# Kernel optimization log

Measured on AMD Instinct MI355X. Metric: run time of the kernel, lower is better.

Reference implementation:

```python
import jax, jax.numpy as jnp
import numpy as np

NUM_SCALES = 3
LAMBDA_0 = 1.0
MU_0 = 1.0
KAPPA_LAMBDA = 0.5
KAPPA_MU = 0.5
BASE_WEIGHT = 1.0
GRADIENT_SCALING = 0.1


def tgradient(f, axis):
    """torch.gradient semantics: central diff interior, one-sided at edges (spacing=1)."""
    n = f.shape[axis]
    def sl(a, b):
        idx = [slice(None)] * f.ndim
        idx[axis] = slice(a, b)
        return f[tuple(idx)]
    interior = (sl(2, n) - sl(0, n - 2)) * 0.5
    first = sl(1, 2) - sl(0, 1)
    last = sl(n - 1, n) - sl(n - 2, n - 1)
    return jnp.concatenate([first, interior, last], axis=axis)


def resize1d_linear(x, axis, out_size):
    """1D linear resize along `axis` with align_corners=True."""
    in_size = x.shape[axis]
    if out_size == in_size:
        return x
    denom = max(out_size - 1, 1)
    coords = jnp.arange(out_size, dtype=jnp.float32) * ((in_size - 1) / denom)
    i0 = jnp.floor(coords).astype(jnp.int32)
    i1 = jnp.minimum(i0 + 1, in_size - 1)
    w = (coords - i0.astype(jnp.float32)).astype(x.dtype)
    shape = [1] * x.ndim
    shape[axis] = out_size
    w = w.reshape(shape)
    x0 = jnp.take(x, i0, axis=axis)
    x1 = jnp.take(x, i1, axis=axis)
    return x0 * (1 - w) + x1 * w


def trilinear_downsample(x, scale):
    # F.interpolate(..., scale_factor=1/scale, mode='trilinear', align_corners=True,
    # recompute_scale_factor=True): out_size = floor(in_size / scale); separable linear.
    for axis in (2, 3, 4):
        out_size = int(np.floor(x.shape[axis] / scale))
        x = resize1d_linear(x, axis, out_size)
    return x


def elasticity_loss(deformation_field, image):
    total_loss = jnp.float32(0.0)
    for i in range(NUM_SCALES):
        scale = 2 ** i
        deform = trilinear_downsample(deformation_field, scale)
        img = trilinear_downsample(image, scale)
        u, v, w = deform[:, 0], deform[:, 1], deform[:, 2]  # each (B, X, Y, Z)
        du_dx, du_dy, du_dz = tgradient(u, 1), tgradient(u, 2), tgradient(u, 3)
        dv_dx, dv_dy, dv_dz = tgradient(v, 1), tgradient(v, 2), tgradient(v, 3)
        dw_dx, dw_dy, dw_dz = tgradient(w, 1), tgradient(w, 2), tgradient(w, 3)
        E_xx, E_yy, E_zz = du_dx, dv_dy, dw_dz
        E_xy = 0.5 * (du_dy + dv_dx)
        E_xz = 0.5 * (du_dz + dw_dx)
        E_yz = 0.5 * (dv_dz + dw_dy)
        trace_E = E_xx + E_yy + E_zz
        ic = img[:, 0]  # (B, X, Y, Z)
        gx, gy, gz = tgradient(ic, 1), tgradient(ic, 2), tgradient(ic, 3)
        image_gradient = jnp.sqrt(gx * gx + gy * gy + gz * gz)
        adaptive_lambda = LAMBDA_0 + KAPPA_LAMBDA * image_gradient
        adaptive_mu = MU_0 + KAPPA_MU * image_gradient
        elastic_energy = (0.5 * adaptive_lambda * trace_E ** 2
                          + adaptive_mu * (E_xx ** 2 + E_yy ** 2 + E_zz ** 2
                                           + 2.0 * (E_xy ** 2 + E_xz ** 2 + E_yz ** 2)))
        adaptive_weight = BASE_WEIGHT + GRADIENT_SCALING * image_gradient
        total_loss = total_loss + jnp.mean(adaptive_weight * elastic_energy)
    return total_loss


def setup_inputs() -> dict:
    key = jax.random.key(0)
    k1, k2 = jax.random.split(key)
    deformation_field = jax.random.normal(k1, (2, 3, 160, 192, 160), dtype=jnp.float32)
    image = jax.random.uniform(k2, (2, 1, 160, 192, 160), dtype=jnp.float32)
    return {"deformation_field": deformation_field, "image": image}


def reference(deformation_field, image):
    return elasticity_loss(deformation_field, image)
```

## Files before the change

kernel.cpp:

```cpp
#include <hip/hip_runtime.h>
#include <math.h>


#define LAMBDA_0 1.0f
#define MU_0 1.0f
#define KAPPA_LAMBDA 0.5f
#define KAPPA_MU 0.5f
#define BASE_WEIGHT 1.0f
#define GRADIENT_SCALING 0.1f

typedef float v4f __attribute__((ext_vector_type(4)));

constexpr int S_TY = 32;
constexpr int S_TZ = 32;
constexpr int S_CX = 8;

__global__ __launch_bounds__(256, 2)
void elasticity_stream_reg2_kernel(const float* __restrict__ def,
                                   const float* __restrict__ img,
                                   int X, int Y, int Z,
                                   int nby, int nbz, int nbx,
                                   float inv_n, float* __restrict__ out) {
    int t = blockIdx.x;
    const int bx = t % nbx; t /= nbx;
    const int bz = t % nbz; t /= nbz;
    const int by = t % nby; t /= nby;
    const int b = t;

    const int tid = threadIdx.x;
    const int zg = tid & 7;
    const int ly = tid >> 3;
    const int lane = tid & 63;
    const int laneM = (lane - 1) & 63;
    const int laneP = (lane + 1) & 63;

    const long long vol = (long long)X * Y * Z;
    const long long sX = (long long)Y * Z;
    const float* __restrict__ p0 = def + ((long long)b * 3 + 0) * vol;
    const float* __restrict__ p1 = def + ((long long)b * 3 + 1) * vol;
    const float* __restrict__ p2 = def + ((long long)b * 3 + 2) * vol;
    const float* __restrict__ p3 = img + (long long)b * vol;

    const int gy = by * S_TY + ly;
    const int gz0 = bz * S_TZ + 4 * zg;
    const int x0 = bx * S_CX;

    const long long offC  = (long long)gy * Z + gz0;
    const long long offYm = (long long)max(gy - 1, 0) * Z + gz0;
    const long long offYp = (long long)min(gy + 1, Y - 1) * Z + gz0;
    const long long offZm = offC - ((gz0 > 0) ? 1 : 0);
    const long long offZp = offC + ((gz0 + 4 < Z) ? 4 : 3);

    const bool ylo = (gy == 0), yhi = (gy == Y - 1);
    const bool zlo = (gz0 == 0), zhi = (gz0 + 4 == Z);
    const bool zem = (zg == 0),  zep = (zg == 7);

    v4f pc[4], cc[4], nc[4];
    {
        const long long o_ = (long long)max(x0 - 1, 0) * sX;
        pc[0] = *(const v4f*)(p0 + o_ + offC);
        pc[1] = *(const v4f*)(p1 + o_ + offC);
        pc[2] = *(const v4f*)(p2 + o_ + offC);
        pc[3] = *(const v4f*)(p3 + o_ + offC);
    }
    {
        const long long o_ = (long long)x0 * sX;
        cc[0] = *(const v4f*)(p0 + o_ + offC);
        cc[1] = *(const v4f*)(p1 + o_ + offC);
        cc[2] = *(const v4f*)(p2 + o_ + offC);
        cc[3] = *(const v4f*)(p3 + o_ + offC);
    }

    float acc = 0.f;
#pragma unroll 2
    for (int i = 0; i < S_CX; ++i) {
        const int x = x0 + i;
        const bool xlo = (x == 0), xhi = (x == X - 1);
        const long long oC = (long long)x * sX;
        const long long oN = (long long)min(x + 1, X - 1) * sX;

        nc[0] = *(const v4f*)(p0 + oN + offC);
        nc[1] = *(const v4f*)(p1 + oN + offC);
        nc[2] = *(const v4f*)(p2 + oN + offC);
        nc[3] = *(const v4f*)(p3 + oN + offC);

        v4f ym[4], yp[4];
        ym[0] = *(const v4f*)(p0 + oC + offYm);
        ym[1] = *(const v4f*)(p1 + oC + offYm);
        ym[2] = *(const v4f*)(p2 + oC + offYm);
        ym[3] = *(const v4f*)(p3 + oC + offYm);
        yp[0] = *(const v4f*)(p0 + oC + offYp);
        yp[1] = *(const v4f*)(p1 + oC + offYp);
        yp[2] = *(const v4f*)(p2 + oC + offYp);
        yp[3] = *(const v4f*)(p3 + oC + offYp);

        float zmS[4] = {0.f, 0.f, 0.f, 0.f};
        float zpS[4] = {0.f, 0.f, 0.f, 0.f};
        if (zem) {
            zmS[0] = p0[oC + offZm]; zmS[1] = p1[oC + offZm];
            zmS[2] = p2[oC + offZm]; zmS[3] = p3[oC + offZm];
        }
        if (zep) {
            zpS[0] = p0[oC + offZp]; zpS[1] = p1[oC + offZp];
            zpS[2] = p2[oC + offZp]; zpS[3] = p3[oC + offZp];
        }

        v4f gxA[4], gyA[4], gzA[4];
#pragma unroll
        for (int f = 0; f < 4; ++f) {
            v4f c = cc[f];
            gxA[f] = xlo ? (nc[f] - c)
                         : (xhi ? (c - pc[f]) : 0.5f * (nc[f] - pc[f]));
            gyA[f] = ylo ? (yp[f] - c)
                         : (yhi ? (c - ym[f]) : 0.5f * (yp[f] - ym[f]));
            float zmv = __shfl(c[3], laneM, 64);
            float zpv = __shfl(c[0], laneP, 64);
            float zm = zem ? zmS[f] : zmv;
            float zp = zep ? zpS[f] : zpv;
            v4f gz;
            gz[0] = zlo ? (c[1] - c[0]) : 0.5f * (c[1] - zm);
            gz[1] = 0.5f * (c[2] - c[0]);
            gz[2] = 0.5f * (c[3] - c[1]);
            gz[3] = zhi ? (c[3] - c[2]) : 0.5f * (zp - c[2]);
            gzA[f] = gz;
        }

#pragma unroll
        for (int j = 0; j < 4; ++j) {
            float Exx = gxA[0][j], Eyy = gyA[1][j], Ezz = gzA[2][j];
            float Exy = 0.5f * (gyA[0][j] + gxA[1][j]);
            float Exz = 0.5f * (gzA[0][j] + gxA[2][j]);
            float Eyz = 0.5f * (gzA[1][j] + gyA[2][j]);
            float tr = Exx + Eyy + Ezz;
            float g = sqrtf(gxA[3][j] * gxA[3][j] + gyA[3][j] * gyA[3][j] +
                            gzA[3][j] * gzA[3][j]);
            float lam = LAMBDA_0 + KAPPA_LAMBDA * g;
            float mu  = MU_0 + KAPPA_MU * g;
            float energy = 0.5f * lam * tr * tr +
                           mu * (Exx * Exx + Eyy * Eyy + Ezz * Ezz +
                                 2.0f * (Exy * Exy + Exz * Exz + Eyz * Eyz));
            acc += (BASE_WEIGHT + GRADIENT_SCALING * g) * energy;
        }

#pragma unroll
        for (int f = 0; f < 4; ++f) { pc[f] = cc[f]; cc[f] = nc[f]; }
    }

    float val = acc * inv_n;
    for (int off = 32; off > 0; off >>= 1)
        val += __shfl_down(val, off, 64);
    __shared__ float smem[4];
    const int wid = (int)(threadIdx.x >> 6);
    if ((threadIdx.x & 63) == 0) smem[wid] = val;
    __syncthreads();
    if (threadIdx.x == 0)
        atomicAdd(out, smem[0] + smem[1] + smem[2] + smem[3]);
}


__global__ void downsample3d_kernel(const float* __restrict__ in,
                                    float* __restrict__ out,
                                    int nmaps,
                                    int inX, int inY, int inZ,
                                    int outX, int outY, int outZ,
                                    float rx, float ry, float rz) {
    long long total = (long long)nmaps * outX * outY * outZ;
    long long idx = (long long)blockIdx.x * blockDim.x + threadIdx.x;
    if (idx >= total) return;

    int z = (int)(idx % outZ);
    long long t = idx / outZ;
    int y = (int)(t % outY);
    t /= outY;
    int x = (int)(t % outX);
    int m = (int)(t / outX);

    float cx = (float)x * rx;
    float cy = (float)y * ry;
    float cz = (float)z * rz;
    int ix0 = (int)floorf(cx), iy0 = (int)floorf(cy), iz0 = (int)floorf(cz);
    float wx = cx - (float)ix0, wy = cy - (float)iy0, wz = cz - (float)iz0;
    int ix1 = min(ix0 + 1, inX - 1);
    int iy1 = min(iy0 + 1, inY - 1);
    int iz1 = min(iz0 + 1, inZ - 1);

    long long sYZ = (long long)inY * inZ;
    const float* p = in + (long long)m * inX * sYZ;

    long long bx0 = (long long)ix0 * sYZ, bx1 = (long long)ix1 * sYZ;
    long long by0 = (long long)iy0 * inZ, by1 = (long long)iy1 * inZ;

    float v000 = p[bx0 + by0 + iz0], v001 = p[bx0 + by0 + iz1];
    float v010 = p[bx0 + by1 + iz0], v011 = p[bx0 + by1 + iz1];
    float v100 = p[bx1 + by0 + iz0], v101 = p[bx1 + by0 + iz1];
    float v110 = p[bx1 + by1 + iz0], v111 = p[bx1 + by1 + iz1];

    float a00 = v000 * (1.f - wx) + v100 * wx;
    float a01 = v001 * (1.f - wx) + v101 * wx;
    float a10 = v010 * (1.f - wx) + v110 * wx;
    float a11 = v011 * (1.f - wx) + v111 * wx;
    float b0 = a00 * (1.f - wy) + a10 * wy;
    float b1 = a01 * (1.f - wy) + a11 * wy;
    out[idx] = b0 * (1.f - wz) + b1 * wz;
}

__global__ void elasticity_loss_v4_kernel(const float* __restrict__ def,
                                          const float* __restrict__ img,
                                          int B, int X, int Y, int Z,
                                          float inv_n,
                                          float* __restrict__ out) {
    const int Zg = Z >> 2;
    long long total = (long long)B * X * Y * Zg;
    long long idx = (long long)blockIdx.x * blockDim.x + threadIdx.x;
    float val = 0.f;
    if (idx < total) {
        int zg = (int)(idx % Zg);
        long long t = idx / Zg;
        int y = (int)(t % Y);
        t /= Y;
        int x = (int)(t % X);
        int b = (int)(t / X);
        int z0 = zg << 2;

        long long vol = (long long)X * Y * Z;
        const float* base0 = def + ((long long)b * 3 + 0) * vol;
        const float* base1 = def + ((long long)b * 3 + 1) * vol;
        const float* base2 = def + ((long long)b * 3 + 2) * vol;
        const float* base3 = img + (long long)b * vol;
        const float* bases[4] = {base0, base1, base2, base3};

        long long sX = (long long)Y * Z;
        long long c = (long long)x * sX + (long long)y * Z + z0;
        long long cxm = (x > 0) ? c - sX : c;
        long long cxp = (x < X - 1) ? c + sX : c;
        long long cym = (y > 0) ? c - Z : c;
        long long cyp = (y < Y - 1) ? c + Z : c;
        long long czm = (z0 > 0) ? c - 1 : c;
        long long czp = (z0 + 4 < Z) ? c + 4 : c;

        float C[4][4], XM[4][4], XP[4][4], YM[4][4], YP[4][4];
        float ZM[4], ZP[4];
#pragma unroll
        for (int f = 0; f < 4; ++f) {
            const float* p = bases[f];
            float4 tc = *(const float4*)(p + c);
            float4 txm = *(const float4*)(p + cxm);
            float4 txp = *(const float4*)(p + cxp);
            float4 tym = *(const float4*)(p + cym);
            float4 typ = *(const float4*)(p + cyp);
            ZM[f] = p[czm];
            ZP[f] = p[czp];
            C[f][0] = tc.x;  C[f][1] = tc.y;  C[f][2] = tc.z;  C[f][3] = tc.w;
            XM[f][0] = txm.x; XM[f][1] = txm.y; XM[f][2] = txm.z; XM[f][3] = txm.w;
            XP[f][0] = txp.x; XP[f][1] = txp.y; XP[f][2] = txp.z; XP[f][3] = txp.w;
            YM[f][0] = tym.x; YM[f][1] = tym.y; YM[f][2] = tym.z; YM[f][3] = tym.w;
            YP[f][0] = typ.x; YP[f][1] = typ.y; YP[f][2] = typ.z; YP[f][3] = typ.w;
        }

        const bool xlo = (x == 0), xhi = (x == X - 1);
        const bool ylo = (y == 0), yhi = (y == Y - 1);
        const bool zlo = (z0 == 0), zhi = (z0 + 4 == Z);

        float GX[4][4], GY[4][4], GZ[4][4];
#pragma unroll
        for (int f = 0; f < 4; ++f) {
#pragma unroll
            for (int i = 0; i < 4; ++i) {
                GX[f][i] = xlo ? (XP[f][i] - C[f][i])
                               : (xhi ? (C[f][i] - XM[f][i])
                                      : 0.5f * (XP[f][i] - XM[f][i]));
                GY[f][i] = ylo ? (YP[f][i] - C[f][i])
                               : (yhi ? (C[f][i] - YM[f][i])
                                      : 0.5f * (YP[f][i] - YM[f][i]));
            }
            GZ[f][0] = zlo ? (C[f][1] - C[f][0]) : 0.5f * (C[f][1] - ZM[f]);
            GZ[f][1] = 0.5f * (C[f][2] - C[f][0]);
            GZ[f][2] = 0.5f * (C[f][3] - C[f][1]);
            GZ[f][3] = zhi ? (C[f][3] - C[f][2]) : 0.5f * (ZP[f] - C[f][2]);
        }

        float acc = 0.f;
#pragma unroll
        for (int i = 0; i < 4; ++i) {
            float Exx = GX[0][i], Eyy = GY[1][i], Ezz = GZ[2][i];
            float Exy = 0.5f * (GY[0][i] + GX[1][i]);
            float Exz = 0.5f * (GZ[0][i] + GX[2][i]);
            float Eyz = 0.5f * (GZ[1][i] + GY[2][i]);
            float tr = Exx + Eyy + Ezz;
            float g = sqrtf(GX[3][i] * GX[3][i] + GY[3][i] * GY[3][i] +
                            GZ[3][i] * GZ[3][i]);
            float lam = LAMBDA_0 + KAPPA_LAMBDA * g;
            float mu  = MU_0 + KAPPA_MU * g;
            float energy = 0.5f * lam * tr * tr +
                           mu * (Exx * Exx + Eyy * Eyy + Ezz * Ezz +
                                 2.0f * (Exy * Exy + Exz * Exz + Eyz * Eyz));
            float wgt = BASE_WEIGHT + GRADIENT_SCALING * g;
            acc += wgt * energy;
        }
        val = acc * inv_n;
    }

    for (int off = 32; off > 0; off >>= 1)
        val += __shfl_down(val, off, 64);
    __shared__ float smem[8];
    int lane = threadIdx.x & 63;
    int wid = (int)(threadIdx.x >> 6);
    if (lane == 0) smem[wid] = val;
    __syncthreads();
    if (threadIdx.x == 0) {
        float s = 0.f;
        int nw = (int)(blockDim.x >> 6);
        for (int i = 0; i < nw; ++i) s += smem[i];
        atomicAdd(out, s);
    }
}

static void launch_loss_v4(const float* def, const float* img, int B, int X,
                           int Y, int Z, float* out, hipStream_t stream) {
    const int BLOCK = 256;
    long long nvox = (long long)B * X * Y * Z;
    long long total = nvox >> 2;
    float inv_n = (float)(1.0 / (double)nvox);
    int grid = (int)((total + BLOCK - 1) / BLOCK);
    elasticity_loss_v4_kernel<<<grid, BLOCK, 0, stream>>>(def, img, B, X, Y, Z,
                                                          inv_n, out);
}

extern "C" void kernel_launch(void* const* d_in, const int* in_sizes, int n_in,
                              void* d_out, int out_size, void* d_ws, size_t ws_size,
                              hipStream_t stream) {
    const float* def = (const float*)d_in[0];
    const float* img = (const float*)d_in[1];
    float* out = (float*)d_out;

    const int B = 2;
    const int X0 = 160, Y0 = 192, Z0 = 160;

    hipMemsetAsync(out, 0, sizeof(float), stream);

    const int BLOCK = 256;

    {
        long long nvox = (long long)B * X0 * Y0 * Z0;
        float inv_n = (float)(1.0 / (double)nvox);
        int nby = Y0 / S_TY;
        int nbz = Z0 / S_TZ;
        int nbx = X0 / S_CX;
        int grid = B * nby * nbz * nbx;
        elasticity_stream_reg2_kernel<<<grid, 256, 0, stream>>>(def, img,
                                                                X0, Y0, Z0,
                                                                nby, nbz, nbx,
                                                                inv_n, out);
    }

    const int X2 = 80, Y2 = 96, Z2 = 80;
    const int X4 = 40, Y4 = 48, Z4 = 40;
    long long vol2 = (long long)X2 * Y2 * Z2;
    long long vol4 = (long long)X4 * Y4 * Z4;

    float* def2 = (float*)d_ws;
    float* img2 = def2 + (long long)B * 3 * vol2;
    float* def4 = img2 + (long long)B * vol2;
    float* img4 = def4 + (long long)B * 3 * vol4;

    {
        float rx = (float)((double)(X0 - 1) / (double)(X2 - 1));
        float ry = (float)((double)(Y0 - 1) / (double)(Y2 - 1));
        float rz = (float)((double)(Z0 - 1) / (double)(Z2 - 1));
        long long td = (long long)B * 3 * vol2;
        int gd = (int)((td + BLOCK - 1) / BLOCK);
        downsample3d_kernel<<<gd, BLOCK, 0, stream>>>(def, def2, B * 3,
                                                      X0, Y0, Z0, X2, Y2, Z2,
                                                      rx, ry, rz);
        long long ti = (long long)B * vol2;
        int gi = (int)((ti + BLOCK - 1) / BLOCK);
        downsample3d_kernel<<<gi, BLOCK, 0, stream>>>(img, img2, B,
                                                      X0, Y0, Z0, X2, Y2, Z2,
                                                      rx, ry, rz);
        launch_loss_v4(def2, img2, B, X2, Y2, Z2, out, stream);
    }

    {
        float rx = (float)((double)(X0 - 1) / (double)(X4 - 1));
        float ry = (float)((double)(Y0 - 1) / (double)(Y4 - 1));
        float rz = (float)((double)(Z0 - 1) / (double)(Z4 - 1));
        long long td = (long long)B * 3 * vol4;
        int gd = (int)((td + BLOCK - 1) / BLOCK);
        downsample3d_kernel<<<gd, BLOCK, 0, stream>>>(def, def4, B * 3,
                                                      X0, Y0, Z0, X4, Y4, Z4,
                                                      rx, ry, rz);
        long long ti = (long long)B * vol4;
        int gi = (int)((ti + BLOCK - 1) / BLOCK);
        downsample3d_kernel<<<gi, BLOCK, 0, stream>>>(img, img4, B,
                                                      X0, Y0, Z0, X4, Y4, Z4,
                                                      rx, ry, rz);
        launch_loss_v4(def4, img4, B, X4, Y4, Z4, out, stream);
    }
}
```

Baseline: 134.8 us.

## Share y-neighbors via wave shuffles, prefetch x+2 plane, merge downsample launches

The full-resolution stencil kernel now takes y-1/y+1 neighbors from adjacent lanes via __shfl and only loads them from global memory for wave-boundary rows. It also prefetches the x+2 plane one iteration ahead, with deeper unrolling and a higher occupancy hint. Separately, the def and img downsample launches at each scale are merged into one kernel covering all 8 maps. The goal is to cut redundant global loads and launch overhead, at the cost of extra shuffle instructions and register pressure that may spill under the tighter launch bounds.

```diff
diff --git a/kernel.cpp b/kernel.cpp
--- a/kernel.cpp
+++ b/kernel.cpp
@@ -15,8 +15,8 @@
 constexpr int S_TZ = 32;
 constexpr int S_CX = 8;
 
-__global__ __launch_bounds__(256, 2)
-void elasticity_stream_reg2_kernel(const float* __restrict__ def,
+__global__ __launch_bounds__(256, 3)
+void elasticity_stream_shfl_kernel(const float* __restrict__ def,
                                    const float* __restrict__ img,
                                    int X, int Y, int Z,
                                    int nby, int nbz, int nbx,
@@ -31,8 +31,11 @@
     const int zg = tid & 7;
     const int ly = tid >> 3;
     const int lane = tid & 63;
+    const int lyw = lane >> 3;
     const int laneM = (lane - 1) & 63;
     const int laneP = (lane + 1) & 63;
+    const int laneYm = (lyw > 0) ? (lane - 8) : lane;
+    const int laneYp = (lyw < 7) ? (lane + 8) : lane;
 
     const long long vol = (long long)X * Y * Z;
     const long long sX = (long long)Y * Z;
@@ -54,8 +57,10 @@
     const bool ylo = (gy == 0), yhi = (gy == Y - 1);
     const bool zlo = (gz0 == 0), zhi = (gz0 + 4 == Z);
     const bool zem = (zg == 0),  zep = (zg == 7);
-
-    v4f pc[4], cc[4], nc[4];
+    const bool yEdgeM = (lyw == 0) && !ylo;
+    const bool yEdgeP = (lyw == 7) && !yhi;
+
+    v4f pc[4], cc[4], nc[4], nn[4];
     {
         const long long o_ = (long long)max(x0 - 1, 0) * sX;
         pc[0] = *(const v4f*)(p0 + o_ + offC);
@@ -70,32 +75,36 @@
         cc[2] = *(const v4f*)(p2 + o_ + offC);
         cc[3] = *(const v4f*)(p3 + o_ + offC);
     }
+    {
+        const long long o_ = (long long)min(x0 + 1, X - 1) * sX;
+        nc[0] = *(const v4f*)(p0 + o_ + offC);
+        nc[1] = *(const v4f*)(p1 + o_ + offC);
+        nc[2] = *(const v4f*)(p2 + o_ + offC);
+        nc[3] = *(const v4f*)(p3 + o_ + offC);
+    }
 
     float acc = 0.f;
-#pragma unroll 2
+#pragma unroll 4
     for (int i = 0; i < S_CX; ++i) {
         const int x = x0 + i;
         const bool xlo = (x == 0), xhi = (x == X - 1);
         const long long oC = (long long)x * sX;
-        const long long oN = (long long)min(x + 1, X - 1) * sX;
-
-        nc[0] = *(const v4f*)(p0 + oN + offC);
-        nc[1] = *(const v4f*)(p1 + oN + offC);
-        nc[2] = *(const v4f*)(p2 + oN + offC);
-        nc[3] = *(const v4f*)(p3 + oN + offC);
-
-        v4f ym[4], yp[4];
-        ym[0] = *(const v4f*)(p0 + oC + offYm);
-        ym[1] = *(const v4f*)(p1 + oC + offYm);
-        ym[2] = *(const v4f*)(p2 + oC + offYm);
-        ym[3] = *(const v4f*)(p3 + oC + offYm);
-        yp[0] = *(const v4f*)(p0 + oC + offYp);
-        yp[1] = *(const v4f*)(p1 + oC + offYp);
-        yp[2] = *(const v4f*)(p2 + oC + offYp);
-        yp[3] = *(const v4f*)(p3 + oC + offYp);
-
-        float zmS[4] = {0.f, 0.f, 0.f, 0.f};
-        float zpS[4] = {0.f, 0.f, 0.f, 0.f};
+        const long long oNN = (long long)min(x + 2, X - 1) * sX;
+
+        v4f ymL[4], ypL[4];
+        if (yEdgeM) {
+            ymL[0] = *(const v4f*)(p0 + oC + offYm);
+            ymL[1] = *(const v4f*)(p1 + oC + offYm);
+            ymL[2] = *(const v4f*)(p2 + oC + offYm);
+            ymL[3] = *(const v4f*)(p3 + oC + offYm);
+        }
+        if (yEdgeP) {
+            ypL[0] = *(const v4f*)(p0 + oC + offYp);
+            ypL[1] = *(const v4f*)(p1 + oC + offYp);
+            ypL[2] = *(const v4f*)(p2 + oC + offYp);
+            ypL[3] = *(const v4f*)(p3 + oC + offYp);
+        }
+        float zmS[4], zpS[4];
         if (zem) {
             zmS[0] = p0[oC + offZm]; zmS[1] = p1[oC + offZm];
             zmS[2] = p2[oC + offZm]; zmS[3] = p3[oC + offZm];
@@ -104,6 +113,10 @@
             zpS[0] = p0[oC + offZp]; zpS[1] = p1[oC + offZp];
             zpS[2] = p2[oC + offZp]; zpS[3] = p3[oC + offZp];
         }
+        nn[0] = *(const v4f*)(p0 + oNN + offC);
+        nn[1] = *(const v4f*)(p1 + oNN + offC);
+        nn[2] = *(const v4f*)(p2 + oNN + offC);
+        nn[3] = *(const v4f*)(p3 + oNN + offC);
 
         v4f gxA[4], gyA[4], gzA[4];
 #pragma unroll
@@ -111,8 +124,18 @@
             v4f c = cc[f];
             gxA[f] = xlo ? (nc[f] - c)
                          : (xhi ? (c - pc[f]) : 0.5f * (nc[f] - pc[f]));
-            gyA[f] = ylo ? (yp[f] - c)
-                         : (yhi ? (c - ym[f]) : 0.5f * (yp[f] - ym[f]));
+
+            v4f ymv, ypv;
+#pragma unroll
+            for (int j = 0; j < 4; ++j) {
+                ymv[j] = __shfl(c[j], laneYm, 64);
+                ypv[j] = __shfl(c[j], laneYp, 64);
+            }
+            if (yEdgeM) ymv = ymL[f];
+            if (yEdgeP) ypv = ypL[f];
+            gyA[f] = ylo ? (ypv - c)
+                         : (yhi ? (c - ymv) : 0.5f * (ypv - ymv));
+
             float zmv = __shfl(c[3], laneM, 64);
             float zpv = __shfl(c[0], laneP, 64);
             float zm = zem ? zmS[f] : zmv;
@@ -143,7 +166,7 @@
         }
 
 #pragma unroll
-        for (int f = 0; f < 4; ++f) { pc[f] = cc[f]; cc[f] = nc[f]; }
+        for (int f = 0; f < 4; ++f) { pc[f] = cc[f]; cc[f] = nc[f]; nc[f] = nn[f]; }
     }
 
     float val = acc * inv_n;
@@ -157,23 +180,30 @@
         atomicAdd(out, smem[0] + smem[1] + smem[2] + smem[3]);
 }
 
-
-__global__ void downsample3d_kernel(const float* __restrict__ in,
-                                    float* __restrict__ out,
-                                    int nmaps,
-                                    int inX, int inY, int inZ,
-                                    int outX, int outY, int outZ,
-                                    float rx, float ry, float rz) {
-    long long total = (long long)nmaps * outX * outY * outZ;
+__global__ void downsample_all8_kernel(const float* __restrict__ def,
+                                       const float* __restrict__ img,
+                                       float* __restrict__ odef,
+                                       float* __restrict__ oimg,
+                                       int inX, int inY, int inZ,
+                                       int outX, int outY, int outZ,
+                                       float rx, float ry, float rz) {
+    long long pervol = (long long)outX * outY * outZ;
+    long long total = 8LL * pervol;
     long long idx = (long long)blockIdx.x * blockDim.x + threadIdx.x;
     if (idx >= total) return;
 
-    int z = (int)(idx % outZ);
-    long long t = idx / outZ;
+    int m = (int)(idx / pervol);
+    long long r = idx % pervol;
+    int z = (int)(r % outZ);
+    long long t = r / outZ;
     int y = (int)(t % outY);
-    t /= outY;
-    int x = (int)(t % outX);
-    int m = (int)(t / outX);
+    int x = (int)(t / outY);
+
+    long long invol = (long long)inX * inY * inZ;
+    const float* src;
+    float* dst;
+    if (m < 6) { src = def + (long long)m * invol;       dst = odef + (long long)m * pervol; }
+    else       { src = img + (long long)(m - 6) * invol; dst = oimg + (long long)(m - 6) * pervol; }
 
     float cx = (float)x * rx;
     float cy = (float)y * ry;
@@ -185,15 +215,13 @@
     int iz1 = min(iz0 + 1, inZ - 1);
 
     long long sYZ = (long long)inY * inZ;
-    const float* p = in + (long long)m * inX * sYZ;
-
     long long bx0 = (long long)ix0 * sYZ, bx1 = (long long)ix1 * sYZ;
     long long by0 = (long long)iy0 * inZ, by1 = (long long)iy1 * inZ;
 
-    float v000 = p[bx0 + by0 + iz0], v001 = p[bx0 + by0 + iz1];
-    float v010 = p[bx0 + by1 + iz0], v011 = p[bx0 + by1 + iz1];
-    float v100 = p[bx1 + by0 + iz0], v101 = p[bx1 + by0 + iz1];
-    float v110 = p[bx1 + by1 + iz0], v111 = p[bx1 + by1 + iz1];
+    float v000 = src[bx0 + by0 + iz0], v001 = src[bx0 + by0 + iz1];
+    float v010 = src[bx0 + by1 + iz0], v011 = src[bx0 + by1 + iz1];
+    float v100 = src[bx1 + by0 + iz0], v101 = src[bx1 + by0 + iz1];
+    float v110 = src[bx1 + by1 + iz0], v111 = src[bx1 + by1 + iz1];
 
     float a00 = v000 * (1.f - wx) + v100 * wx;
     float a01 = v001 * (1.f - wx) + v101 * wx;
@@ -201,7 +229,7 @@
     float a11 = v011 * (1.f - wx) + v111 * wx;
     float b0 = a00 * (1.f - wy) + a10 * wy;
     float b1 = a01 * (1.f - wy) + a11 * wy;
-    out[idx] = b0 * (1.f - wz) + b1 * wz;
+    dst[r] = b0 * (1.f - wz) + b1 * wz;
 }
 
 __global__ void elasticity_loss_v4_kernel(const float* __restrict__ def,
@@ -347,7 +375,7 @@
         int nbz = Z0 / S_TZ;
         int nbx = X0 / S_CX;
         int grid = B * nby * nbz * nbx;
-        elasticity_stream_reg2_kernel<<<grid, 256, 0, stream>>>(def, img,
+        elasticity_stream_shfl_kernel<<<grid, 256, 0, stream>>>(def, img,
                                                                 X0, Y0, Z0,
                                                                 nby, nbz, nbx,
                                                                 inv_n, out);
@@ -367,16 +395,11 @@
         float rx = (float)((double)(X0 - 1) / (double)(X2 - 1));
         float ry = (float)((double)(Y0 - 1) / (double)(Y2 - 1));
         float rz = (float)((double)(Z0 - 1) / (double)(Z2 - 1));
-        long long td = (long long)B * 3 * vol2;
-        int gd = (int)((td + BLOCK - 1) / BLOCK);
-        downsample3d_kernel<<<gd, BLOCK, 0, stream>>>(def, def2, B * 3,
-                                                      X0, Y0, Z0, X2, Y2, Z2,
-                                                      rx, ry, rz);
-        long long ti = (long long)B * vol2;
-        int gi = (int)((ti + BLOCK - 1) / BLOCK);
-        downsample3d_kernel<<<gi, BLOCK, 0, stream>>>(img, img2, B,
-                                                      X0, Y0, Z0, X2, Y2, Z2,
-                                                      rx, ry, rz);
+        long long total = 8LL * vol2;
+        int g = (int)((total + BLOCK - 1) / BLOCK);
+        downsample_all8_kernel<<<g, BLOCK, 0, stream>>>(def, img, def2, img2,
+                                                        X0, Y0, Z0, X2, Y2, Z2,
+                                                        rx, ry, rz);
         launch_loss_v4(def2, img2, B, X2, Y2, Z2, out, stream);
     }
 
@@ -384,16 +407,11 @@
         float rx = (float)((double)(X0 - 1) / (double)(X4 - 1));
         float ry = (float)((double)(Y0 - 1) / (double)(Y4 - 1));
         float rz = (float)((double)(Z0 - 1) / (double)(Z4 - 1));
-        long long td = (long long)B * 3 * vol4;
-        int gd = (int)((td + BLOCK - 1) / BLOCK);
-        downsample3d_kernel<<<gd, BLOCK, 0, stream>>>(def, def4, B * 3,
-                                                      X0, Y0, Z0, X4, Y4, Z4,
-                                                      rx, ry, rz);
-        long long ti = (long long)B * vol4;
-        int gi = (int)((ti + BLOCK - 1) / BLOCK);
-        downsample3d_kernel<<<gi, BLOCK, 0, stream>>>(img, img4, B,
-                                                      X0, Y0, Z0, X4, Y4, Z4,
-                                                      rx, ry, rz);
+        long long total = 8LL * vol4;
+        int g = (int)((total + BLOCK - 1) / BLOCK);
+        downsample_all8_kernel<<<g, BLOCK, 0, stream>>>(def, img, def4, img4,
+                                                        X0, Y0, Z0, X4, Y4, Z4,
+                                                        rx, ry, rz);
         launch_loss_v4(def4, img4, B, X4, Y4, Z4, out, stream);
     }
 }
```

Measured after the change: 508.5 us. 277% more time.
